# Performance work log

Hardware: AMD Instinct MI355X
Metric: run time of the kernel (lower is better)

The kernel has to match this reference:

```python
import jax, jax.numpy as jnp
import numpy as np

GROUPS = 32
EPS = 1e-6


def group_norm(x, scale, bias):
    B, C, H, W = x.shape
    xg = x.reshape(B, GROUPS, C // GROUPS, H, W)
    mean = xg.mean(axis=(2, 3, 4), keepdims=True)
    var = xg.var(axis=(2, 3, 4), keepdims=True)
    xg = (xg - mean) * jax.lax.rsqrt(var + EPS)
    x = xg.reshape(B, C, H, W)
    return x * scale[None, :, None, None] + bias[None, :, None, None]


def conv1x1(x, w, b):
    # x: [B,C,H,W], w: [O,C], b: [O]
    return jnp.einsum('bchw,oc->bohw', x, w) + b[None, :, None, None]


def setup_inputs() -> dict:
    key = jax.random.key(0)
    ks = jax.random.split(key, 6)
    B, C, H, W = 8, 256, 64, 64
    s = 1.0 / np.sqrt(C)
    return {
        'x': jax.random.normal(ks[0], (B, C, H, W), dtype=jnp.float32),
        'gn_scale': jnp.ones((C,), dtype=jnp.float32),
        'gn_bias': jnp.zeros((C,), dtype=jnp.float32),
        'wq': jax.random.normal(ks[1], (C, C), dtype=jnp.float32) * s,
        'bq': jnp.zeros((C,), dtype=jnp.float32),
        'wk': jax.random.normal(ks[2], (C, C), dtype=jnp.float32) * s,
        'bk': jnp.zeros((C,), dtype=jnp.float32),
        'wv': jax.random.normal(ks[3], (C, C), dtype=jnp.float32) * s,
        'bv': jnp.zeros((C,), dtype=jnp.float32),
        'wo': jax.random.normal(ks[4], (C, C), dtype=jnp.float32) * s,
        'bo': jnp.zeros((C,), dtype=jnp.float32),
    }


def reference(x, gn_scale, gn_bias, wq, bq, wk, bk, wv, bv, wo, bo):
    skip = x
    h = group_norm(x, gn_scale, gn_bias)
    B, C, H, W = h.shape
    N = H * W
    q = conv1x1(h, wq, bq).reshape(B, C, N)  # [B,C,N]
    k = conv1x1(h, wk, bk).reshape(B, C, N)
    v = conv1x1(h, wv, bv).reshape(B, C, N)
    # scores[b,i,j] = sum_c q[b,c,i] k[b,c,j] / sqrt(C)
    scores = jnp.einsum('bci,bcj->bij', q, k) / jnp.sqrt(jnp.float32(C))
    a = jax.nn.softmax(scores, axis=2)  # softmax over keys j
    # z[b,c,i] = sum_j v[b,c,j] a[b,i,j]
    z = jnp.einsum('bcj,bij->bci', v, a).reshape(B, C, H, W)
    z = conv1x1(z, wo, bo)
    return skip + z
```

## Files before the change

kernel.cpp:

```cpp
#include <hip/hip_runtime.h>
#include <math.h>

typedef __bf16 bf16;
typedef __bf16 bf16x8 __attribute__((ext_vector_type(8)));
typedef __bf16 bf16x4 __attribute__((ext_vector_type(4)));
typedef float  f32x4  __attribute__((ext_vector_type(4)));
typedef float  f32x16 __attribute__((ext_vector_type(16)));
typedef unsigned int u32;
typedef unsigned char u8;
typedef u32 u32x2 __attribute__((ext_vector_type(2)));
typedef u32 u32x4 __attribute__((ext_vector_type(4)));
typedef int  i32x8 __attribute__((ext_vector_type(8)));

#define MFMA(a, b, c)   __builtin_amdgcn_mfma_f32_16x16x32_bf16((a), (b), (c), 0, 0, 0)
#define MFMAS(a, b, c)                                                           \
  __builtin_amdgcn_mfma_scale_f32_32x32x64_f8f6f4((a), (b), (c), 0, 0,           \
                                                  0, 0x7f7f7f7f, 0, 0x7f7f7f7f)

#define GLOAD_LDS16(g, l)                                                        \
  __builtin_amdgcn_global_load_lds(                                              \
      (const __attribute__((address_space(1))) void*)(g),                        \
      (__attribute__((address_space(3))) void*)(l), 16, 0, 0)

static constexpr int B_ = 8, C_ = 256, N_ = 4096;
static constexpr float QSCALE = 0.09016844005556021f;
static constexpr float PBIAS  = 2.0f;

static constexpr size_t HT_OFF = 0;
static constexpr size_t QT_OFF = 16777216;
static constexpr size_t KT_OFF = 25165824;
static constexpr size_t V_OFF  = 33554432;
static constexpr size_t WQ_OFF = 41943040;
static constexpr size_t WK_OFF = WQ_OFF + 131072;
static constexpr size_t WV_OFF = WK_OFF + 131072;
static constexpr size_t WO_OFF = WV_OFF + 131072;
static constexpr size_t LS_OFF = WO_OFF + 131072;
static constexpr size_t ZN2_OFF = LS_OFF + 524288;
static constexpr size_t PART_ELEMS = (size_t)B_ * C_ * N_;

__global__ __launch_bounds__(256) void wconv_kernel(
    const float* __restrict__ wq, const float* __restrict__ wk,
    const float* __restrict__ wv, const float* __restrict__ wo,
    bf16* __restrict__ oq, bf16* __restrict__ ok, bf16* __restrict__ ov, bf16* __restrict__ oo) {
  int i = blockIdx.x * 256 + threadIdx.x;
  oq[i] = (bf16)wq[i];
  ok[i] = (bf16)wk[i];
  ov[i] = (bf16)wv[i];
  oo[i] = (bf16)wo[i];
}

__global__ __launch_bounds__(512) void gn_kernel(
    const float* __restrict__ x, const float* __restrict__ gsc, const float* __restrict__ gbi,
    bf16* __restrict__ hT) {
  int b = blockIdx.x >> 5, g = blockIdx.x & 31, c0 = g * 8;
  int t = threadIdx.x;
  const float* base = x + ((size_t)(b * C_ + c0)) * N_;
  __shared__ bf16 xl[32768];
  float s = 0.f, ss = 0.f;
  const f32x4* b4 = (const f32x4*)base;
#pragma unroll
  for (int p = 0; p < 16; p++) {
    int u = t + p * 512;
    f32x4 v = b4[u];
    s  += v[0] + v[1] + v[2] + v[3];
    ss += v[0] * v[0] + v[1] * v[1] + v[2] * v[2] + v[3] * v[3];
    bf16x4 xv;
#pragma unroll
    for (int e = 0; e < 4; e++) xv[e] = (bf16)v[e];
    *(bf16x4*)(xl + u * 4) = xv;
  }
#pragma unroll
  for (int off = 1; off < 64; off <<= 1) {
    s  += __shfl_xor(s, off);
    ss += __shfl_xor(ss, off);
  }
  __shared__ float red[16];
  if ((t & 63) == 0) { red[(t >> 6) * 2] = s; red[(t >> 6) * 2 + 1] = ss; }
  __syncthreads();
  s = 0.f; ss = 0.f;
#pragma unroll
  for (int r = 0; r < 8; r++) { s += red[r * 2]; ss += red[r * 2 + 1]; }
  float mean = s * (1.f / 32768.f);
  float var  = ss * (1.f / 32768.f) - mean * mean;
  float rstd = rsqrtf(var + 1e-6f);
  float aa[8], bb[8];
#pragma unroll
  for (int cc = 0; cc < 8; cc++) {
    aa[cc] = rstd * gsc[c0 + cc];
    bb[cc] = gbi[c0 + cc] - mean * aa[cc];
  }
#pragma unroll
  for (int ii = 0; ii < 8; ii++) {
    int i = t + ii * 512;
    bf16x8 o;
#pragma unroll
    for (int cc = 0; cc < 8; cc++) o[cc] = (bf16)((float)xl[cc * 4096 + i] * aa[cc] + bb[cc]);
    *(bf16x8*)(hT + ((size_t)(b * N_ + i)) * C_ + c0) = o;
  }
}

__global__ __launch_bounds__(256) void qkv_kernel(
    const bf16* __restrict__ hT,
    const bf16* __restrict__ wqb, const bf16* __restrict__ wkb, const bf16* __restrict__ wvb,
    const float* __restrict__ bq, const float* __restrict__ bk, const float* __restrict__ bv,
    u8* __restrict__ qT8, u8* __restrict__ kT8, u8* __restrict__ v8) {
  int b = blockIdx.x >> 6, i0 = (blockIdx.x & 63) << 6;
  int t = threadIdx.x, w = t >> 6, lane = t & 63, quad = lane >> 4, l15 = lane & 15;
  __shared__ bf16 hl[64 * 264];
#pragma unroll
  for (int p = 0; p < 8; p++) {
    int u = t + p * 256, r = u >> 5, c16 = u & 31;
    *(bf16x8*)(hl + r * 264 + c16 * 8) =
        *(const bf16x8*)(hT + ((size_t)(b * N_ + i0 + r)) * C_ + c16 * 8);
  }
  __syncthreads();
  int cw0 = w * 64;

  f32x4 aq[4][4], ak[4][4];
#pragma unroll
  for (int a = 0; a < 4; a++)
#pragma unroll
    for (int bb2 = 0; bb2 < 4; bb2++) { aq[a][bb2] = (f32x4){0.f,0.f,0.f,0.f}; ak[a][bb2] = (f32x4){0.f,0.f,0.f,0.f}; }
  for (int kc = 0; kc < 8; kc++) {
    bf16x8 hb[4];
#pragma unroll
    for (int it = 0; it < 4; it++)
      hb[it] = *(const bf16x8*)(hl + (it * 16 + l15) * 264 + kc * 32 + quad * 8);
#pragma unroll
    for (int ct = 0; ct < 4; ct++) {
      bf16x8 wqf = *(const bf16x8*)(wqb + ((size_t)(cw0 + ct * 16 + l15)) * C_ + kc * 32 + quad * 8);
      bf16x8 wkf = *(const bf16x8*)(wkb + ((size_t)(cw0 + ct * 16 + l15)) * C_ + kc * 32 + quad * 8);
#pragma unroll
      for (int it = 0; it < 4; it++) {
        aq[ct][it] = MFMA(wqf, hb[it], aq[ct][it]);
        ak[ct][it] = MFMA(wkf, hb[it], ak[ct][it]);
      }
    }
  }
#pragma unroll
  for (int ct = 0; ct < 4; ct++)
#pragma unroll
    for (int it = 0; it < 4; it++) {
      int c4 = cw0 + ct * 16 + quad * 4;
      int i  = i0 + it * 16 + l15;
      f32x4 bq4 = *(const f32x4*)(bq + c4);
      f32x4 bk4 = *(const f32x4*)(bk + c4);
      float qv[4], kv[4];
#pragma unroll
      for (int r = 0; r < 4; r++) {
        qv[r] = (aq[ct][it][r] + bq4[r]) * (QSCALE * 4.0f);
        kv[r] = (ak[ct][it][r] + bk4[r]) * 0.25f;
      }
      u32 qd = (u32)__builtin_amdgcn_cvt_pk_fp8_f32(qv[0], qv[1], 0, false);
      qd = (u32)__builtin_amdgcn_cvt_pk_fp8_f32(qv[2], qv[3], (int)qd, true);
      u32 kd = (u32)__builtin_amdgcn_cvt_pk_fp8_f32(kv[0], kv[1], 0, false);
      kd = (u32)__builtin_amdgcn_cvt_pk_fp8_f32(kv[2], kv[3], (int)kd, true);
      *(u32*)(qT8 + ((size_t)(b * N_ + i)) * C_ + c4) = qd;
      *(u32*)(kT8 + ((size_t)(b * N_ + i)) * C_ + c4) = kd;
    }

  f32x4 av[4][4];
#pragma unroll
  for (int a = 0; a < 4; a++)
#pragma unroll
    for (int bb2 = 0; bb2 < 4; bb2++) av[a][bb2] = (f32x4){0.f,0.f,0.f,0.f};
  for (int kc = 0; kc < 8; kc++) {
    bf16x8 ha[4];
#pragma unroll
    for (int it = 0; it < 4; it++)
      ha[it] = *(const bf16x8*)(hl + (it * 16 + l15) * 264 + kc * 32 + quad * 8);
#pragma unroll
    for (int ct = 0; ct < 4; ct++) {
      bf16x8 wvf = *(const bf16x8*)(wvb + ((size_t)(cw0 + ct * 16 + l15)) * C_ + kc * 32 + quad * 8);
#pragma unroll
      for (int it = 0; it < 4; it++) av[it][ct] = MFMA(ha[it], wvf, av[it][ct]);
    }
  }
#pragma unroll
  for (int it = 0; it < 4; it++)
#pragma unroll
    for (int ct = 0; ct < 4; ct++) {
      int c  = cw0 + ct * 16 + l15;
      int i4 = i0 + it * 16 + quad * 4;
      float bvc = bv[c];
      float vv4[4];
#pragma unroll
      for (int r = 0; r < 4; r++) vv4[r] = av[it][ct][r] + bvc;
      u32 vd = (u32)__builtin_amdgcn_cvt_pk_fp8_f32(vv4[0], vv4[1], 0, false);
      vd = (u32)__builtin_amdgcn_cvt_pk_fp8_f32(vv4[2], vv4[3], (int)vd, true);
      *(u32*)(v8 + ((size_t)(b * C_ + c)) * N_ + i4) = vd;
    }
}

__global__ __launch_bounds__(256, 2) void attn_kernel(
    const u8* __restrict__ qT8, const u8* __restrict__ kT8, const u8* __restrict__ v8,
    bf16* __restrict__ zn0, bf16* __restrict__ znR, float* __restrict__ lsum) {
  constexpr int NJT = 32;
  int blk = blockIdx.x;
  int sp = blk >> 8;
  int b = blk & 7;
  int i0 = ((blk >> 3) & 31) << 7;
  int t = threadIdx.x, w = t >> 6, lane = t & 63;
  int r31 = lane & 31, h = lane >> 5;
  __shared__ __align__(16) u8 lds8[4 * 16384];

  int iw = i0 + w * 32;
  const u8* qrow = qT8 + ((size_t)(b * N_ + iw + r31)) * C_ + h * 32;
  i32x8 qB[4];
#pragma unroll
  for (int m = 0; m < 4; m++) qB[m] = *(const i32x8*)(qrow + m * 64);

  f32x16 of[8];
#pragma unroll
  for (int ct = 0; ct < 8; ct++)
#pragma unroll
    for (int e = 0; e < 16; e++) of[ct][e] = 0.f;
  float lacc = 0.f;

  int ks = r31 & 7;
  int kr_off = lane >> 4;
  int kc_pos = lane & 15;
  int vr_off = lane >> 2;
  int vc_pos = lane & 3;
  int spBase = sp * 2048;

  auto stageK = [&](int jts, u8* kb) {
    int j0s = spBase + jts * 64;
#pragma unroll
    for (int p = 0; p < 4; p++) {
      int idx = w * 4 + p;
      int r = idx * 4 + kr_off;
      int chunk = kc_pos ^ (r & 7);
      GLOAD_LDS16(kT8 + ((size_t)(b * N_ + j0s + r)) * C_ + chunk * 16, kb + idx * 1024);
    }
  };
  auto stageV = [&](int jts, u8* vb) {
    int j0s = spBase + jts * 64;
#pragma unroll
    for (int p = 0; p < 4; p++) {
      int idx = w * 4 + p;
      int c = idx * 16 + vr_off;
      int chunk = vc_pos ^ ((c >> 1) & 3);
      GLOAD_LDS16(v8 + ((size_t)(b * C_ + c)) * N_ + j0s + chunk * 16, vb + idx * 1024);
    }
  };

  stageK(0, lds8);
  stageV(0, lds8 + 32768);

  if (__popc(blk) & 1) __builtin_amdgcn_s_sleep(48);

  i32x8 pPrev;

  for (int jt = 0; jt < NJT; jt++) {
    stageK(jt < NJT - 1 ? jt + 1 : jt, lds8 + (((jt + 1) & 1) << 14));
    asm volatile("s_waitcnt vmcnt(8)" ::: "memory");
    __builtin_amdgcn_s_barrier();
    const u8* kTl = lds8 + ((jt & 1) << 14);
    const u8* vbp = lds8 + 32768 + (((jt + 1) & 1) << 14);

    f32x16 st0;
#pragma unroll
    for (int e = 0; e < 16; e++) st0[e] = -PBIAS;
    {
      const u8* krow = kTl + r31 * 256;
      __builtin_amdgcn_s_setprio(1);
#pragma unroll
      for (int m = 0; m < 4; m++) {
        int cd = m * 4 + h * 2;
        union { i32x8 v; u32x4 h4[2]; } kf;
        kf.h4[0] = *(const u32x4*)(krow + ((cd ^ ks) * 16));
        kf.h4[1] = *(const u32x4*)(krow + (((cd + 1) ^ ks) * 16));
        st0 = MFMAS(kf.v, qB[m], st0);
      }
    }
    if (jt) {
#pragma unroll
      for (int ct = 0; ct < 8; ct++) {
        int c = ct * 32 + r31;
        int vs = (c >> 1) & 3;
        const u8* vrow = vbp + c * 64;
        union { i32x8 v; u32x4 h4[2]; } vB;
        vB.h4[0] = *(const u32x4*)(vrow + (((2 * h) ^ vs) * 16));
        vB.h4[1] = *(const u32x4*)(vrow + (((2 * h + 1) ^ vs) * 16));
        of[ct] = MFMAS(pPrev, vB.v, of[ct]);
      }
    }
    __builtin_amdgcn_s_setprio(0);
    u32 PG0[4], PG1[4];
#pragma unroll
    for (int b4 = 0; b4 < 4; b4++) {
      float p0 = __builtin_amdgcn_exp2f(st0[b4 * 4 + 0]);
      float p1 = __builtin_amdgcn_exp2f(st0[b4 * 4 + 1]);
      float p2 = __builtin_amdgcn_exp2f(st0[b4 * 4 + 2]);
      float p3 = __builtin_amdgcn_exp2f(st0[b4 * 4 + 3]);
      lacc += (p0 + p1) + (p2 + p3);
      u32 d = (u32)__builtin_amdgcn_cvt_pk_fp8_f32(p0, p1, 0, false);
      d = (u32)__builtin_amdgcn_cvt_pk_fp8_f32(p2, p3, (int)d, true);
      PG0[b4] = d;
    }
    f32x16 st1;
#pragma unroll
    for (int e = 0; e < 16; e++) st1[e] = -PBIAS;
    {
      const u8* krow = kTl + (32 + r31) * 256;
      __builtin_amdgcn_s_setprio(1);
#pragma unroll
      for (int m = 0; m < 4; m++) {
        int cd = m * 4 + h * 2;
        union { i32x8 v; u32x4 h4[2]; } kf;
        kf.h4[0] = *(const u32x4*)(krow + ((cd ^ ks) * 16));
        kf.h4[1] = *(const u32x4*)(krow + (((cd + 1) ^ ks) * 16));
        st1 = MFMAS(kf.v, qB[m], st1);
      }
      __builtin_amdgcn_s_setprio(0);
    }
#pragma unroll
    for (int b4 = 0; b4 < 4; b4++) {
      float p0 = __builtin_amdgcn_exp2f(st1[b4 * 4 + 0]);
      float p1 = __builtin_amdgcn_exp2f(st1[b4 * 4 + 1]);
      float p2 = __builtin_amdgcn_exp2f(st1[b4 * 4 + 2]);
      float p3 = __builtin_amdgcn_exp2f(st1[b4 * 4 + 3]);
      lacc += (p0 + p1) + (p2 + p3);
      u32 d = (u32)__builtin_amdgcn_cvt_pk_fp8_f32(p0, p1, 0, false);
      d = (u32)__builtin_amdgcn_cvt_pk_fp8_f32(p2, p3, (int)d, true);
      PG1[b4] = d;
    }
#pragma unroll
    for (int b4 = 0; b4 < 4; b4++) {
      u32x2 rr = __builtin_amdgcn_permlane32_swap(PG0[b4], PG1[b4], false, false);
      pPrev[2 * b4]     = (int)rr[0];
      pPrev[2 * b4 + 1] = (int)rr[1];
    }

    __builtin_amdgcn_s_barrier();
    if (jt < NJT - 1) stageV(jt + 1, lds8 + 32768 + (((jt + 1) & 1) << 14));
  }

  asm volatile("s_waitcnt vmcnt(0)" ::: "memory");
  __builtin_amdgcn_s_barrier();
  {
    const u8* vbp = lds8 + 32768 + (((NJT - 1) & 1) << 14);
#pragma unroll
    for (int ct = 0; ct < 8; ct++) {
      int c = ct * 32 + r31;
      int vs = (c >> 1) & 3;
      const u8* vrow = vbp + c * 64;
      union { i32x8 v; u32x4 h4[2]; } vB;
      vB.h4[0] = *(const u32x4*)(vrow + (((2 * h) ^ vs) * 16));
      vB.h4[1] = *(const u32x4*)(vrow + (((2 * h + 1) ^ vs) * 16));
      of[ct] = MFMAS(pPrev, vB.v, of[ct]);
    }
  }

  lacc += __shfl_xor(lacc, 32);
  if (h == 0)
    lsum[((size_t)(sp * 8 + b)) * N_ + iw + r31] = lacc;
  bf16* zn = (sp == 0) ? zn0 : znR;
#pragma unroll
  for (int ct = 0; ct < 8; ct++) {
    int c = ct * 32 + r31;
#pragma unroll
    for (int g = 0; g < 4; g++) {
      bf16x4 zv;
#pragma unroll
      for (int e = 0; e < 4; e++) zv[e] = (bf16)of[ct][g * 4 + e];
      int i4 = iw + 8 * g + 4 * h;
      *(bf16x4*)(zn + ((size_t)(b * C_ + c)) * N_ + i4) = zv;
    }
  }
}

__global__ __launch_bounds__(256) void combine_kernel(
    const bf16* __restrict__ zn0, const bf16* __restrict__ znR,
    const float* __restrict__ lsum,
    const bf16* __restrict__ wob, const float* __restrict__ bo,
    const float* __restrict__ x, float* __restrict__ out) {
  int b = blockIdx.x >> 6, i0 = (blockIdx.x & 63) << 6;
  int t = threadIdx.x, w = t >> 6, lane = t & 63, quad = lane >> 4, l15 = lane & 15;
  __shared__ bf16 zl[64 * 264];
  __shared__ float linv[64];

  if (t < 64) {
    size_t ii = (size_t)b * N_ + i0 + t;
    linv[t] = 1.f / (lsum[ii] + lsum[ii + (size_t)8 * N_]);
  }
  __syncthreads();

#pragma unroll
  for (int p = 0; p < 16; p++) {
    int u = t + p * 256, c = u >> 4, ii = (u & 15) * 4;
    size_t base = ((size_t)(b * C_ + c)) * N_ + i0 + ii;
    bf16x4 z0 = *(const bf16x4*)(zn0 + base);
    bf16x4 z1 = *(const bf16x4*)(znR + base);
#pragma unroll
    for (int e = 0; e < 4; e++)
      zl[(ii + e) * 264 + c] = (bf16)(((float)z0[e] + (float)z1[e]) * linv[ii + e]);
  }
  __syncthreads();

  f32x4 oa[4][4];
#pragma unroll
  for (int a = 0; a < 4; a++)
#pragma unroll
    for (int bb2 = 0; bb2 < 4; bb2++) oa[a][bb2] = (f32x4){0.f, 0.f, 0.f, 0.f};
  for (int kc = 0; kc < 8; kc++) {
    bf16x8 za[4];
#pragma unroll
    for (int it = 0; it < 4; it++)
      za[it] = *(const bf16x8*)(zl + (it * 16 + l15) * 264 + kc * 32 + quad * 8);
#pragma unroll
    for (int ctl = 0; ctl < 4; ctl++) {
      bf16x8 wf = *(const bf16x8*)(wob + ((size_t)(w * 64 + ctl * 16 + l15)) * C_ + kc * 32 + quad * 8);
#pragma unroll
      for (int it = 0; it < 4; it++) oa[ctl][it] = MFMA(za[it], wf, oa[ctl][it]);
    }
  }
#pragma unroll
  for (int ctl = 0; ctl < 4; ctl++)
#pragma unroll
    for (int it = 0; it < 4; it++) {
      int c = w * 64 + ctl * 16 + l15;
      size_t base = ((size_t)(b * C_ + c)) * N_ + i0 + it * 16 + quad * 4;
      f32x4 xs = *(const f32x4*)(x + base);
      float boc = bo[c];
      f32x4 o4;
#pragma unroll
      for (int r = 0; r < 4; r++) o4[r] = oa[ctl][it][r] + boc + xs[r];
      *(f32x4*)(out + base) = o4;
    }
}

extern "C" void kernel_launch(void* const* d_in, const int* in_sizes, int n_in,
                              void* d_out, int out_size, void* d_ws, size_t ws_size,
                              hipStream_t stream) {
  const float* x   = (const float*)d_in[0];
  const float* gsc = (const float*)d_in[1];
  const float* gbi = (const float*)d_in[2];
  const float* wq  = (const float*)d_in[3];
  const float* bq  = (const float*)d_in[4];
  const float* wk  = (const float*)d_in[5];
  const float* bk  = (const float*)d_in[6];
  const float* wv  = (const float*)d_in[7];
  const float* bv  = (const float*)d_in[8];
  const float* wo  = (const float*)d_in[9];
  const float* bo  = (const float*)d_in[10];

  char* ws = (char*)d_ws;
  bf16* hT   = (bf16*)(ws + HT_OFF);
  u8*   qT8  = (u8*)(ws + QT_OFF);
  u8*   kT8  = (u8*)(ws + KT_OFF);
  u8*   v8   = (u8*)(ws + V_OFF);
  bf16* wqb  = (bf16*)(ws + WQ_OFF);
  bf16* wkb  = (bf16*)(ws + WK_OFF);
  bf16* wvb  = (bf16*)(ws + WV_OFF);
  bf16* wob  = (bf16*)(ws + WO_OFF);
  float* lsum = (float*)(ws + LS_OFF);
  bf16* zn0  = (bf16*)(ws + HT_OFF);
  bf16* znR  = (bf16*)(ws + ZN2_OFF);

  wconv_kernel<<<256, 256, 0, stream>>>(wq, wk, wv, wo, wqb, wkb, wvb, wob);
  gn_kernel<<<256, 512, 0, stream>>>(x, gsc, gbi, hT);
  qkv_kernel<<<512, 256, 0, stream>>>(hT, wqb, wkb, wvb, bq, bk, bv, qT8, kT8, v8);
  attn_kernel<<<512, 256, 0, stream>>>(qT8, kT8, v8, zn0, znR, lsum);
  combine_kernel<<<512, 256, 0, stream>>>(zn0, znR, lsum, wob, bo, x, (float*)d_out);
}
```

Baseline: 247.9 us.

## Stage QKV fp8 outputs through swizzled LDS for coalesced stores, fuse weight conversion

The weight bf16 conversion kernel is folded into the group-norm kernel, which removes one launch. The QKV epilogue now writes the fp8 q, k and v tiles into an XOR-swizzled LDS buffer and then issues 16-byte coalesced global stores, replacing the scattered 4-byte stores. The combine kernel's LDS row stride changes from 264 to 266 to reduce bank conflicts on the transposed writes. This costs extra LDS space and several barriers in the QKV kernel.

```diff
diff --git a/kernel.cpp b/kernel.cpp
--- a/kernel.cpp
+++ b/kernel.cpp
@@ -38,22 +38,21 @@
 static constexpr size_t ZN2_OFF = LS_OFF + 524288;
 static constexpr size_t PART_ELEMS = (size_t)B_ * C_ * N_;
 
-__global__ __launch_bounds__(256) void wconv_kernel(
+__global__ __launch_bounds__(512) void gn_kernel(
+    const float* __restrict__ x, const float* __restrict__ gsc, const float* __restrict__ gbi,
+    bf16* __restrict__ hT,
     const float* __restrict__ wq, const float* __restrict__ wk,
     const float* __restrict__ wv, const float* __restrict__ wo,
     bf16* __restrict__ oq, bf16* __restrict__ ok, bf16* __restrict__ ov, bf16* __restrict__ oo) {
-  int i = blockIdx.x * 256 + threadIdx.x;
-  oq[i] = (bf16)wq[i];
-  ok[i] = (bf16)wk[i];
-  ov[i] = (bf16)wv[i];
-  oo[i] = (bf16)wo[i];
-}
-
-__global__ __launch_bounds__(512) void gn_kernel(
-    const float* __restrict__ x, const float* __restrict__ gsc, const float* __restrict__ gbi,
-    bf16* __restrict__ hT) {
   int b = blockIdx.x >> 5, g = blockIdx.x & 31, c0 = g * 8;
   int t = threadIdx.x;
+  if (t < 256) {
+    int i = blockIdx.x * 256 + t;
+    oq[i] = (bf16)wq[i];
+    ok[i] = (bf16)wk[i];
+    ov[i] = (bf16)wv[i];
+    oo[i] = (bf16)wo[i];
+  }
   const float* base = x + ((size_t)(b * C_ + c0)) * N_;
   __shared__ bf16 xl[32768];
   float s = 0.f, ss = 0.f;
@@ -107,6 +106,7 @@
   int b = blockIdx.x >> 6, i0 = (blockIdx.x & 63) << 6;
   int t = threadIdx.x, w = t >> 6, lane = t & 63, quad = lane >> 4, l15 = lane & 15;
   __shared__ bf16 hl[64 * 264];
+  __shared__ __align__(16) u8 ep[16384];
 #pragma unroll
   for (int p = 0; p < 8; p++) {
     int u = t + p * 256, r = u >> 5, c16 = u & 31;
@@ -137,27 +137,51 @@
       }
     }
   }
+
 #pragma unroll
   for (int ct = 0; ct < 4; ct++)
 #pragma unroll
     for (int it = 0; it < 4; it++) {
       int c4 = cw0 + ct * 16 + quad * 4;
-      int i  = i0 + it * 16 + l15;
+      int il = it * 16 + l15;
       f32x4 bq4 = *(const f32x4*)(bq + c4);
-      f32x4 bk4 = *(const f32x4*)(bk + c4);
-      float qv[4], kv[4];
-#pragma unroll
-      for (int r = 0; r < 4; r++) {
-        qv[r] = (aq[ct][it][r] + bq4[r]) * (QSCALE * 4.0f);
-        kv[r] = (ak[ct][it][r] + bk4[r]) * 0.25f;
-      }
+      float qv[4];
+#pragma unroll
+      for (int r = 0; r < 4; r++) qv[r] = (aq[ct][it][r] + bq4[r]) * (QSCALE * 4.0f);
       u32 qd = (u32)__builtin_amdgcn_cvt_pk_fp8_f32(qv[0], qv[1], 0, false);
       qd = (u32)__builtin_amdgcn_cvt_pk_fp8_f32(qv[2], qv[3], (int)qd, true);
+      *(u32*)(ep + il * 256 + ((((c4 >> 4) ^ (il & 15)) << 4) | (c4 & 12))) = qd;
+    }
+  __syncthreads();
+#pragma unroll
+  for (int p = 0; p < 4; p++) {
+    int u = p * 256 + t, il = u >> 4, ch = u & 15;
+    *(u32x4*)(qT8 + ((size_t)(b * N_ + i0 + il)) * C_ + ch * 16) =
+        *(const u32x4*)(ep + il * 256 + (((ch ^ (il & 15)) << 4)));
+  }
+  __syncthreads();
+
+#pragma unroll
+  for (int ct = 0; ct < 4; ct++)
+#pragma unroll
+    for (int it = 0; it < 4; it++) {
+      int c4 = cw0 + ct * 16 + quad * 4;
+      int il = it * 16 + l15;
+      f32x4 bk4 = *(const f32x4*)(bk + c4);
+      float kv[4];
+#pragma unroll
+      for (int r = 0; r < 4; r++) kv[r] = (ak[ct][it][r] + bk4[r]) * 0.25f;
       u32 kd = (u32)__builtin_amdgcn_cvt_pk_fp8_f32(kv[0], kv[1], 0, false);
       kd = (u32)__builtin_amdgcn_cvt_pk_fp8_f32(kv[2], kv[3], (int)kd, true);
-      *(u32*)(qT8 + ((size_t)(b * N_ + i)) * C_ + c4) = qd;
-      *(u32*)(kT8 + ((size_t)(b * N_ + i)) * C_ + c4) = kd;
-    }
+      *(u32*)(ep + il * 256 + ((((c4 >> 4) ^ (il & 15)) << 4) | (c4 & 12))) = kd;
+    }
+  __syncthreads();
+#pragma unroll
+  for (int p = 0; p < 4; p++) {
+    int u = p * 256 + t, il = u >> 4, ch = u & 15;
+    *(u32x4*)(kT8 + ((size_t)(b * N_ + i0 + il)) * C_ + ch * 16) =
+        *(const u32x4*)(ep + il * 256 + (((ch ^ (il & 15)) << 4)));
+  }
 
   f32x4 av[4][4];
 #pragma unroll
@@ -176,20 +200,28 @@
       for (int it = 0; it < 4; it++) av[it][ct] = MFMA(ha[it], wvf, av[it][ct]);
     }
   }
+  __syncthreads();
+
 #pragma unroll
   for (int it = 0; it < 4; it++)
 #pragma unroll
     for (int ct = 0; ct < 4; ct++) {
-      int c  = cw0 + ct * 16 + l15;
-      int i4 = i0 + it * 16 + quad * 4;
-      float bvc = bv[c];
+      int cl = cw0 + ct * 16 + l15;
+      float bvc = bv[cl];
       float vv4[4];
 #pragma unroll
       for (int r = 0; r < 4; r++) vv4[r] = av[it][ct][r] + bvc;
       u32 vd = (u32)__builtin_amdgcn_cvt_pk_fp8_f32(vv4[0], vv4[1], 0, false);
       vd = (u32)__builtin_amdgcn_cvt_pk_fp8_f32(vv4[2], vv4[3], (int)vd, true);
-      *(u32*)(v8 + ((size_t)(b * C_ + c)) * N_ + i4) = vd;
-    }
+      *(u32*)(ep + cl * 64 + ((((it ^ (cl & 3)) << 4)) | (quad * 4))) = vd;
+    }
+  __syncthreads();
+#pragma unroll
+  for (int p = 0; p < 4; p++) {
+    int u = p * 256 + t, cl = u >> 2, io = u & 3;
+    *(u32x4*)(v8 + ((size_t)(b * C_ + cl)) * N_ + i0 + io * 16) =
+        *(const u32x4*)(ep + cl * 64 + (((io ^ (cl & 3)) << 4)));
+  }
 }
 
 __global__ __launch_bounds__(256, 2) void attn_kernel(
@@ -378,7 +410,7 @@
     const float* __restrict__ x, float* __restrict__ out) {
   int b = blockIdx.x >> 6, i0 = (blockIdx.x & 63) << 6;
   int t = threadIdx.x, w = t >> 6, lane = t & 63, quad = lane >> 4, l15 = lane & 15;
-  __shared__ bf16 zl[64 * 264];
+  __shared__ bf16 zl[64 * 266];
   __shared__ float linv[64];
 
   if (t < 64) {
@@ -395,7 +427,7 @@
     bf16x4 z1 = *(const bf16x4*)(znR + base);
 #pragma unroll
     for (int e = 0; e < 4; e++)
-      zl[(ii + e) * 264 + c] = (bf16)(((float)z0[e] + (float)z1[e]) * linv[ii + e]);
+      zl[(ii + e) * 266 + c] = (bf16)(((float)z0[e] + (float)z1[e]) * linv[ii + e]);
   }
   __syncthreads();
 
@@ -408,7 +440,7 @@
     bf16x8 za[4];
 #pragma unroll
     for (int it = 0; it < 4; it++)
-      za[it] = *(const bf16x8*)(zl + (it * 16 + l15) * 264 + kc * 32 + quad * 8);
+      za[it] = *(const bf16x8*)(zl + (it * 16 + l15) * 266 + kc * 32 + quad * 8);
 #pragma unroll
     for (int ctl = 0; ctl < 4; ctl++) {
       bf16x8 wf = *(const bf16x8*)(wob + ((size_t)(w * 64 + ctl * 16 + l15)) * C_ + kc * 32 + quad * 8);
@@ -459,8 +491,7 @@
   bf16* zn0  = (bf16*)(ws + HT_OFF);
   bf16* znR  = (bf16*)(ws + ZN2_OFF);
 
-  wconv_kernel<<<256, 256, 0, stream>>>(wq, wk, wv, wo, wqb, wkb, wvb, wob);
-  gn_kernel<<<256, 512, 0, stream>>>(x, gsc, gbi, hT);
+  gn_kernel<<<256, 512, 0, stream>>>(x, gsc, gbi, hT, wq, wk, wv, wo, wqb, wkb, wvb, wob);
   qkv_kernel<<<512, 256, 0, stream>>>(hT, wqb, wkb, wvb, bq, bk, bv, qT8, kT8, v8);
   attn_kernel<<<512, 256, 0, stream>>>(qT8, kT8, v8, zn0, znR, lsum);
   combine_kernel<<<512, 256, 0, stream>>>(zn0, znR, lsum, wob, bo, x, (float*)d_out);
```

New measurement: 243.5 us. Within noise of the previous version (-1.8%).
